# Performance work log

Hardware: AMD Instinct MI355X
Metric: run time of the kernel (lower is better)

Reference implementation:

```python
import jax, jax.numpy as jnp
import numpy as np

B, D, H = 1024, 1024, 4096  # batch, input_dim, hidden_dim
EPS = 1e-3  # keras LayerNormalization default epsilon


def layer_norm(x, gamma, beta):
    m = jnp.mean(x, axis=-1, keepdims=True)
    v = jnp.var(x, axis=-1, keepdims=True)
    return (x - m) * jax.lax.rsqrt(v + EPS) * gamma + beta


def setup_inputs() -> dict:
    key = jax.random.key(0)
    ks = jax.random.split(key, 8)
    C = D + H  # concat width for gate/FFN projections
    s_in = 0.02
    return {
        "x": jax.random.normal(ks[0], (B, D), jnp.float32),
        "hidden_state": jax.random.normal(ks[1], (B, H), jnp.float32),
        "W_u": jax.random.normal(ks[2], (C, H), jnp.float32) * s_in,
        "b_u": jnp.zeros((H,), jnp.float32),
        "W_r": jax.random.normal(ks[3], (C, H), jnp.float32) * s_in,
        "b_r": jnp.zeros((H,), jnp.float32),
        "W_g": jax.random.normal(ks[4], (C, H), jnp.float32) * s_in,
        "b_g": jnp.zeros((H,), jnp.float32),
        "W_up": jax.random.normal(ks[5], (C, H), jnp.float32) * s_in,
        "b_up": jnp.zeros((H,), jnp.float32),
        "W_d": jax.random.normal(ks[6], (H, D), jnp.float32) * s_in,
        "b_d": jnp.zeros((D,), jnp.float32),
        "gamma_h": jnp.ones((H,), jnp.float32),
        "beta_h": jnp.zeros((H,), jnp.float32),
        "gamma_o": jnp.ones((D,), jnp.float32),
        "beta_o": jnp.zeros((D,), jnp.float32),
    }


def reference(x, hidden_state, W_u, b_u, W_r, b_r, W_g, b_g, W_up, b_up,
              W_d, b_d, gamma_h, beta_h, gamma_o, beta_o):
    h = hidden_state
    combined = jnp.concatenate([x, h], axis=-1)          # [B, D+H]
    u = jax.nn.sigmoid(combined @ W_u + b_u)             # update gate [B, H]
    r = jax.nn.sigmoid(combined @ W_r + b_r)             # reset gate  [B, H]
    cand = jnp.concatenate([x, r * h], axis=-1)          # [B, D+H]
    gate = cand @ W_g + b_g
    up = cand @ W_up + b_up
    swiglu = jax.nn.silu(gate) * up                      # [B, H]
    new_h = layer_norm((1.0 - u) * h + u * swiglu + h, gamma_h, beta_h)
    out = layer_norm(new_h @ W_d + b_d, gamma_o, beta_o)  # [B, D]
    return out, new_h
```

## Files before the change

kernel.cpp:

```cpp
#include <hip/hip_runtime.h>
#include <hip/hip_bf16.h>
#include <math.h>


typedef unsigned short u16;
typedef unsigned int u32;
typedef __attribute__((ext_vector_type(8))) short short8;
typedef __attribute__((ext_vector_type(4))) float floatx4;

#define B_ROWS 1024
#define H_DIM 4096
#define D_DIM 1024
#define LDA_S 72

__device__ __forceinline__ float bf2f(u16 v) {
  u32 u = ((u32)v) << 16;
  return __builtin_bit_cast(float, u);
}
__device__ __forceinline__ u16 f2bf(float f) {
  u32 u = __builtin_bit_cast(u32, f);
  u32 r = (u + 0x7fffu + ((u >> 16) & 1u)) >> 16;
  return (u16)r;
}
__device__ __forceinline__ u32 pkbf(float lo, float hi) {
  return (u32)f2bf(lo) | ((u32)f2bf(hi) << 16);
}

__device__ __forceinline__ void gload_lds16(const u16* g, u16* l) {
  __builtin_amdgcn_global_load_lds(
      (const __attribute__((address_space(1))) void*)g,
      (__attribute__((address_space(3))) void*)l, 16, 0, 0);
}


__launch_bounds__(256)
__global__ void conv_w_k(const float* __restrict__ W0, const float* __restrict__ W1,
                         u16* __restrict__ img, int ldb, int KT, int nbHalf) {
  const int nb = blockIdx.x;
  const int kt = blockIdx.y;
  const float* W = (nb < nbHalf) ? W0 : W1;
  const int nbl = (nb < nbHalf) ? nb : (nb - nbHalf);
  const float* src = W + (size_t)kt * 64 * ldb + (size_t)nbl * 128;
  u16* dst = img + ((size_t)nb * KT + kt) * 8192;
  const int t = threadIdx.x;
  const int n = t & 127;
  const int half = t >> 7;
#pragma unroll
  for (int pass = 0; pass < 4; ++pass) {
    const int kc = half * 4 + pass;
    const float* sp = src + (size_t)(kc * 8) * ldb + n;
    uint4 o;
    o.x = pkbf(sp[0],                 sp[(size_t)ldb]);
    o.y = pkbf(sp[(size_t)2 * ldb],   sp[(size_t)3 * ldb]);
    o.z = pkbf(sp[(size_t)4 * ldb],   sp[(size_t)5 * ldb]);
    o.w = pkbf(sp[(size_t)6 * ldb],   sp[(size_t)7 * ldb]);
    *(uint4*)(dst + (size_t)(kc * 128 + n) * 8) = o;
  }
}

__launch_bounds__(256)
__global__ void conv_xh_k(const float* __restrict__ x, const float* __restrict__ h,
                          u16* __restrict__ imgX, u16* __restrict__ imgH) {
  const int kt = blockIdx.x;
  const int mb = blockIdx.y;
  const float* src;
  u16* dst;
  int lda;
  if (kt < 16) {
    lda = 1024;
    src = x + (size_t)mb * 128 * lda + (size_t)kt * 64;
    dst = imgX + ((size_t)mb * 16 + kt) * 8192;
  } else {
    lda = 4096;
    src = h + (size_t)mb * 128 * lda + (size_t)(kt - 16) * 64;
    dst = imgH + ((size_t)mb * 64 + (kt - 16)) * 8192;
  }
  const int t = threadIdx.x;
  const int j = t & 127;
  const int half = t >> 7;
  const float* sp = src + (size_t)j * lda + half * 32;
#pragma unroll
  for (int pass = 0; pass < 4; ++pass) {
    const int kc = half * 4 + pass;
    const float4 a = *(const float4*)(sp + pass * 8);
    const float4 b = *(const float4*)(sp + pass * 8 + 4);
    uint4 o;
    o.x = pkbf(a.x, a.y);
    o.y = pkbf(a.z, a.w);
    o.z = pkbf(b.x, b.y);
    o.w = pkbf(b.z, b.w);
    *(uint4*)(dst + (size_t)(kc * 128 + j) * 8) = o;
  }
}

template <int MODE>
__launch_bounds__(256)
__global__ void gemm_img(const u16* __restrict__ A0, const u16* __restrict__ A1,
                         const u16* __restrict__ Bimg,
                         const float* __restrict__ bias0, const float* __restrict__ bias1,
                         const float* __restrict__ hglob,
                         float* __restrict__ outF, u16* __restrict__ outB0,
                         u16* __restrict__ outB1) {
  constexpr int KT = (MODE == 3) ? 16 : 80;
  constexpr int KSPLIT = 16;
  constexpr int KT_B = (MODE == 3) ? 64 : 80;

  const int bx = blockIdx.x;
  const int by = blockIdx.y;
  const int kz = (MODE == 3) ? (int)blockIdx.z * 16 : 0;
  const int n0 = bx * 128;
  const int m0 = by * 128;
  const bool second = (MODE != 3) && (n0 >= 4096);
  const int ncol0 = second ? (n0 - 4096) : n0;

  __shared__ __align__(16) u16 As[2][8192];
  __shared__ __align__(16) u16 Bs[2][8192];

  const int t = threadIdx.x;
  const int w = t >> 6;
  const int lane = t & 63;
  const int q = lane >> 4;
  const int i16 = lane & 15;
  const int wm = (w >> 1) * 64;
  const int wn = (w & 1) * 64;

  floatx4 acc[4][4] = {};

  const u16* btile = Bimg + ((size_t)bx * KT_B + kz) * 8192;

  auto stage = [&](int kt, int buf) {
    const u16* a;
    if (MODE == 3) {
      a = A0 + ((size_t)by * 64 + kz + kt) * 8192;
    } else {
      a = (kt < KSPLIT) ? A0 + ((size_t)by * 16 + kt) * 8192
                        : A1 + ((size_t)by * 64 + (kt - KSPLIT)) * 8192;
    }
    const u16* b = btile + (size_t)kt * 8192;
    u16* As_ = &As[buf][0];
    u16* Bs_ = &Bs[buf][0];
#pragma unroll
    for (int i = 0; i < 4; ++i) {
      const int ch = (i * 4 + w) * 512;
      gload_lds16(a + ch + lane * 8, As_ + ch);
      gload_lds16(b + ch + lane * 8, Bs_ + ch);
    }
  };

  stage(0, 0);
  __syncthreads();
  int cur = 0;

  for (int kt = 0; kt < KT; ++kt) {
    if (kt + 1 < KT) stage(kt + 1, cur ^ 1);
#pragma unroll
    for (int s = 0; s < 2; ++s) {
      const int c = s * 4 + q;
      short8 av[4], bv[4];
#pragma unroll
      for (int tm = 0; tm < 4; ++tm)
        av[tm] = *(const short8*)(&As[cur][(size_t)(c * 128 + wm + tm * 16 + i16) * 8]);
#pragma unroll
      for (int tn = 0; tn < 4; ++tn)
        bv[tn] = *(const short8*)(&Bs[cur][(size_t)(c * 128 + wn + tn * 16 + i16) * 8]);
#pragma unroll
      for (int tm = 0; tm < 4; ++tm)
#pragma unroll
        for (int tn = 0; tn < 4; ++tn)
          acc[tm][tn] = __builtin_amdgcn_mfma_f32_16x16x32_bf16(av[tm], bv[tn], acc[tm][tn], 0, 0, 0);
    }
    __syncthreads();
    cur ^= 1;
  }

  const float* __restrict__ biasP = second ? bias1 : bias0;
  float* __restrict__ outP = (MODE == 3) ? outF + (size_t)blockIdx.z * (1024 * 1024) : outF;
#pragma unroll
  for (int tm = 0; tm < 4; ++tm) {
#pragma unroll
    for (int tn = 0; tn < 4; ++tn) {
      const int nloc = ncol0 + wn + tn * 16 + i16;
      const float b = (MODE == 3) ? 0.f : biasP[nloc];
      const int mbase = m0 + wm + tm * 16 + q * 4;
#pragma unroll
      for (int r = 0; r < 4; ++r) {
        const int m = mbase + r;
        const float v = acc[tm][tn][r] + b;
        if (MODE == 1) {
          const float sg = 1.f / (1.f + __expf(-v));
          if (!second) {
            outF[(size_t)m * 4096 + nloc] = sg;
          } else {
            const float rh = sg * hglob[(size_t)m * 4096 + nloc];
            const size_t tb = ((size_t)(m >> 7) * 64 + (nloc >> 6)) * 8192;
            outB0[tb + (size_t)((((nloc >> 3) & 7) * 128) + (m & 127)) * 8 + (nloc & 7)] = f2bf(rh);
          }
        } else if (MODE == 2) {
          if (!second) outB0[(size_t)m * 4096 + nloc] = f2bf(v);
          else         outB1[(size_t)m * 4096 + nloc] = f2bf(v);
        } else {
          outP[(size_t)m * 1024 + nloc] = v;
        }
      }
    }
  }
}

template <int MODE>
__launch_bounds__(256)
__global__ void gemm_k(const float* __restrict__ Af0, const float* __restrict__ Af1,
                       const u16* __restrict__ Ab,
                       const float* __restrict__ Bg0, const float* __restrict__ Bg1,
                       const float* __restrict__ bias0, const float* __restrict__ bias1,
                       const float* __restrict__ hglob,
                       float* __restrict__ outF, u16* __restrict__ outB0,
                       u16* __restrict__ outB1) {
  constexpr int K_TOT = (MODE == 3) ? 4096 : 5120;
  constexpr int KT = K_TOT / 64;
  constexpr int LDB = (MODE == 3) ? 1024 : 4096;

  const int n0 = blockIdx.x * 128;
  const int m0 = blockIdx.y * 128;
  const bool second = (MODE != 3) && (n0 >= 4096);
  const float* __restrict__ Bg = second ? Bg1 : Bg0;
  const int ncol0 = second ? (n0 - 4096) : n0;

  __shared__ __align__(16) u16 As[128 * LDA_S];
  __shared__ __align__(16) u16 Bs[64 * 128];

  const int t = threadIdx.x;
  const int w = t >> 6;
  const int lane = t & 63;
  const int q = lane >> 4;
  const int i16 = lane & 15;
  const int wm = (w >> 1) * 64;
  const int wn = (w & 1) * 64;

  floatx4 acc[4][4] = {};

  for (int kt = 0; kt < KT; ++kt) {
    const int k0 = kt * 64;
    const bool a_is_bf16 = (MODE == 2) && (k0 >= 1024);
    if (a_is_bf16) {
      const u16* Ag = Ab;
      const int lda = 4096;
      const int krel = k0 - 1024;
#pragma unroll
      for (int c = 0; c < 4; ++c) {
        const int p = c * 256 + t;
        const int row = p >> 3;
        const int cp = p & 7;
        const uint4 v = *(const uint4*)(Ag + (size_t)(m0 + row) * lda + krel + cp * 8);
        *(uint4*)(&As[row * LDA_S + cp * 8]) = v;
      }
    } else {
      const float* Ag;
      int lda, krel;
      if (MODE == 3)      { Ag = Af0; lda = 4096; krel = k0; }
      else if (k0 < 1024) { Ag = Af0; lda = 1024; krel = k0; }
      else                { Ag = Af1; lda = 4096; krel = k0 - 1024; }
#pragma unroll
      for (int c = 0; c < 8; ++c) {
        const int p = c * 256 + t;
        const int row = p >> 4;
        const int cp = p & 15;
        const float4 v = *(const float4*)(Ag + (size_t)(m0 + row) * lda + krel + cp * 4);
        ushort4 o;
        o.x = f2bf(v.x); o.y = f2bf(v.y); o.z = f2bf(v.z); o.w = f2bf(v.w);
        *(ushort4*)(&As[row * LDA_S + cp * 4]) = o;
      }
    }
#pragma unroll
    for (int cc = 0; cc < 2; ++cc) {
      const int c = 2 * w + cc;
      const float* bp = Bg + (size_t)(k0 + c * 8) * LDB + ncol0;
#pragma unroll
      for (int hn = 0; hn < 2; ++hn) {
        const int n = lane + hn * 64;
        const float* src = bp + n;
        u32 p0 = (u32)f2bf(src[0 * LDB]) | ((u32)f2bf(src[1 * LDB]) << 16);
        u32 p1 = (u32)f2bf(src[2 * LDB]) | ((u32)f2bf(src[3 * LDB]) << 16);
        u32 p2 = (u32)f2bf(src[4 * LDB]) | ((u32)f2bf(src[5 * LDB]) << 16);
        u32 p3 = (u32)f2bf(src[6 * LDB]) | ((u32)f2bf(src[7 * LDB]) << 16);
        *(uint4*)(&Bs[(size_t)(c * 128 + n) * 8]) = make_uint4(p0, p1, p2, p3);
      }
    }
    __syncthreads();
#pragma unroll
    for (int s = 0; s < 2; ++s) {
      short8 av[4], bv[4];
#pragma unroll
      for (int tm = 0; tm < 4; ++tm) {
        const int r = wm + tm * 16 + i16;
        av[tm] = *(const short8*)(&As[r * LDA_S + (s * 4 + q) * 8]);
      }
#pragma unroll
      for (int tn = 0; tn < 4; ++tn) {
        const int n = wn + tn * 16 + i16;
        const int c = s * 4 + q;
        bv[tn] = *(const short8*)(&Bs[(size_t)(c * 128 + n) * 8]);
      }
#pragma unroll
      for (int tm = 0; tm < 4; ++tm)
#pragma unroll
        for (int tn = 0; tn < 4; ++tn)
          acc[tm][tn] = __builtin_amdgcn_mfma_f32_16x16x32_bf16(av[tm], bv[tn], acc[tm][tn], 0, 0, 0);
    }
    __syncthreads();
  }

  const float* __restrict__ biasP = second ? bias1 : bias0;
  constexpr int LDO = (MODE == 3) ? 1024 : 4096;
#pragma unroll
  for (int tm = 0; tm < 4; ++tm) {
#pragma unroll
    for (int tn = 0; tn < 4; ++tn) {
      const int nloc = ncol0 + wn + tn * 16 + i16;
      const float b = biasP[nloc];
      const int mbase = m0 + wm + tm * 16 + q * 4;
#pragma unroll
      for (int r = 0; r < 4; ++r) {
        const int m = mbase + r;
        const float v = acc[tm][tn][r] + b;
        const size_t oidx = (size_t)m * LDO + nloc;
        if (MODE == 1) {
          const float sg = 1.f / (1.f + __expf(-v));
          if (!second) outF[oidx] = sg;
          else         outB0[oidx] = f2bf(sg * hglob[oidx]);
        } else if (MODE == 2) {
          if (!second) outB0[oidx] = f2bf(v);
          else         outB1[oidx] = f2bf(v);
        } else {
          outF[oidx] = v;
        }
      }
    }
  }
}

__launch_bounds__(256)
__global__ void ln_h_k(const float* u_f, const u16* __restrict__ wsg,
                       const u16* __restrict__ wsup, const float* __restrict__ h,
                       const float* __restrict__ gamma, const float* __restrict__ beta,
                       float* out, u16* __restrict__ imgNH) {
  const int row = blockIdx.x, t = threadIdx.x;
  const size_t base = (size_t)row * H_DIM;
  const int i0 = t * 16;
  float tv[16];
  float s = 0.f, s2 = 0.f;
#pragma unroll
  for (int j = 0; j < 16; ++j) {
    const int idx = i0 + j;
    const float u = u_f[base + idx];
    const float g = bf2f(wsg[base + idx]);
    const float up = bf2f(wsup[base + idx]);
    const float hh = h[base + idx];
    const float sw = (g / (1.f + __expf(-g))) * up;
    const float x = (2.f - u) * hh + u * sw;
    tv[j] = x; s += x; s2 += x * x;
  }
#pragma unroll
  for (int off = 32; off; off >>= 1) {
    s += __shfl_down(s, off);
    s2 += __shfl_down(s2, off);
  }
  __shared__ float red[8];
  const int w = t >> 6, lane = t & 63;
  if (lane == 0) { red[w] = s; red[4 + w] = s2; }
  __syncthreads();
  const float S = red[0] + red[1] + red[2] + red[3];
  const float S2 = red[4] + red[5] + red[6] + red[7];
  const float mean = S * (1.f / (float)H_DIM);
  const float var = fmaxf(S2 * (1.f / (float)H_DIM) - mean * mean, 0.f);
  const float rstd = rsqrtf(var + 1e-3f);
#pragma unroll
  for (int cc = 0; cc < 2; ++cc) {
    float o[8];
#pragma unroll
    for (int jj = 0; jj < 8; ++jj) {
      const int idx = i0 + cc * 8 + jj;
      o[jj] = (tv[cc * 8 + jj] - mean) * rstd * gamma[idx] + beta[idx];
      out[base + idx] = o[jj];
    }
    if (imgNH) {
      const int idx8 = i0 + cc * 8;
      uint4 v;
      v.x = pkbf(o[0], o[1]);
      v.y = pkbf(o[2], o[3]);
      v.z = pkbf(o[4], o[5]);
      v.w = pkbf(o[6], o[7]);
      *(uint4*)(&imgNH[((size_t)(row >> 7) * 64 + (idx8 >> 6)) * 8192 +
                       (size_t)((((idx8 >> 3) & 7) * 128) + (row & 127)) * 8]) = v;
    }
  }
}

__launch_bounds__(256)
__global__ void ln_o_k(const float* __restrict__ part, const float* __restrict__ bias,
                       const float* __restrict__ gamma, const float* __restrict__ beta,
                       float* __restrict__ out) {
  const int row = blockIdx.x, t = threadIdx.x;
  const size_t base = (size_t)row * D_DIM;
  const int i0 = t * 4;
  constexpr size_t PSTRIDE = (size_t)1024 * 1024;
  float tv[4];
  float s = 0.f, s2 = 0.f;
#pragma unroll
  for (int j = 0; j < 4; ++j) {
    const size_t idx = base + i0 + j;
    const float x = part[idx] + part[idx + PSTRIDE] + part[idx + 2 * PSTRIDE] +
                    part[idx + 3 * PSTRIDE] + bias[i0 + j];
    tv[j] = x; s += x; s2 += x * x;
  }
#pragma unroll
  for (int off = 32; off; off >>= 1) {
    s += __shfl_down(s, off);
    s2 += __shfl_down(s2, off);
  }
  __shared__ float red[8];
  const int w = t >> 6, lane = t & 63;
  if (lane == 0) { red[w] = s; red[4 + w] = s2; }
  __syncthreads();
  const float S = red[0] + red[1] + red[2] + red[3];
  const float S2 = red[4] + red[5] + red[6] + red[7];
  const float mean = S * (1.f / (float)D_DIM);
  const float var = fmaxf(S2 * (1.f / (float)D_DIM) - mean * mean, 0.f);
  const float rstd = rsqrtf(var + 1e-3f);
#pragma unroll
  for (int j = 0; j < 4; ++j) {
    const int idx = i0 + j;
    out[base + idx] = (tv[j] - mean) * rstd * gamma[idx] + beta[idx];
  }
}

__launch_bounds__(256)
__global__ void ln_o_fb(float* io, const float* __restrict__ gamma,
                        const float* __restrict__ beta) {
  const int row = blockIdx.x, t = threadIdx.x;
  const size_t base = (size_t)row * D_DIM;
  const int i0 = t * 4;
  float tv[4];
  float s = 0.f, s2 = 0.f;
#pragma unroll
  for (int j = 0; j < 4; ++j) {
    const float x = io[base + i0 + j];
    tv[j] = x; s += x; s2 += x * x;
  }
#pragma unroll
  for (int off = 32; off; off >>= 1) {
    s += __shfl_down(s, off);
    s2 += __shfl_down(s2, off);
  }
  __shared__ float red[8];
  const int w = t >> 6, lane = t & 63;
  if (lane == 0) { red[w] = s; red[4 + w] = s2; }
  __syncthreads();
  const float S = red[0] + red[1] + red[2] + red[3];
  const float S2 = red[4] + red[5] + red[6] + red[7];
  const float mean = S * (1.f / (float)D_DIM);
  const float var = fmaxf(S2 * (1.f / (float)D_DIM) - mean * mean, 0.f);
  const float rstd = rsqrtf(var + 1e-3f);
#pragma unroll
  for (int j = 0; j < 4; ++j) {
    const int idx = i0 + j;
    io[base + idx] = (tv[j] - mean) * rstd * gamma[idx] + beta[idx];
  }
}

extern "C" void kernel_launch(void* const* d_in, const int* in_sizes, int n_in,
                              void* d_out, int out_size, void* d_ws, size_t ws_size,
                              hipStream_t stream) {
  (void)in_sizes; (void)n_in; (void)out_size;
  const float* x       = (const float*)d_in[0];
  const float* h       = (const float*)d_in[1];
  const float* W_u     = (const float*)d_in[2];
  const float* b_u     = (const float*)d_in[3];
  const float* W_r     = (const float*)d_in[4];
  const float* b_r     = (const float*)d_in[5];
  const float* W_g     = (const float*)d_in[6];
  const float* b_g     = (const float*)d_in[7];
  const float* W_up    = (const float*)d_in[8];
  const float* b_up    = (const float*)d_in[9];
  const float* W_d     = (const float*)d_in[10];
  const float* b_d     = (const float*)d_in[11];
  const float* gamma_h = (const float*)d_in[12];
  const float* beta_h  = (const float*)d_in[13];
  const float* gamma_o = (const float*)d_in[14];
  const float* beta_o  = (const float*)d_in[15];

  float* out_final = (float*)d_out;
  float* out_newh  = (float*)d_out + (size_t)B_ROWS * D_DIM;
  float* u_buf = out_newh;
  float* o_pre = out_final;

  dim3 blk(256);

  const size_t SZ_W  = (size_t)64 * 80 * 16384;
  const size_t SZ_X  = (size_t)8 * 16 * 16384;
  const size_t SZ_H  = (size_t)8 * 64 * 16384;
  const size_t SZ_RH = SZ_H;
  const size_t SZ_G  = (size_t)B_ROWS * H_DIM * 2;
  const size_t SZ_UP = SZ_G;
  const size_t NEED  = SZ_W + SZ_X + SZ_H + SZ_RH + SZ_G + SZ_UP;

  if (ws_size >= NEED) {
    char* ws = (char*)d_ws;
    u16* imgW  = (u16*)(ws);
    u16* imgX  = (u16*)(ws + SZ_W);
    u16* imgH  = (u16*)(ws + SZ_W + SZ_X);
    u16* imgNH = imgH;
    u16* imgRH = (u16*)(ws + SZ_W + SZ_X + SZ_H);
    u16* ws_g  = (u16*)(ws + SZ_W + SZ_X + SZ_H + SZ_RH);
    u16* ws_up = (u16*)(ws + SZ_W + SZ_X + SZ_H + SZ_RH + SZ_G);
    float* part = (float*)ws_g;

    conv_xh_k<<<dim3(80, 8), blk, 0, stream>>>(x, h, imgX, imgH);
    conv_w_k<<<dim3(64, 80), blk, 0, stream>>>(W_u, W_r, imgW, 4096, 80, 32);
    gemm_img<1><<<dim3(64, 8), blk, 0, stream>>>(imgX, imgH, imgW, b_u, b_r, h,
                                                 u_buf, imgRH, nullptr);
    conv_w_k<<<dim3(64, 80), blk, 0, stream>>>(W_g, W_up, imgW, 4096, 80, 32);
    gemm_img<2><<<dim3(64, 8), blk, 0, stream>>>(imgX, imgRH, imgW, b_g, b_up, nullptr,
                                                 nullptr, ws_g, ws_up);
    ln_h_k<<<dim3(B_ROWS), blk, 0, stream>>>(u_buf, ws_g, ws_up, h, gamma_h, beta_h,
                                             out_newh, imgNH);
    conv_w_k<<<dim3(8, 64), blk, 0, stream>>>(W_d, nullptr, imgW, 1024, 64, 8);
    gemm_img<3><<<dim3(8, 8, 4), blk, 0, stream>>>(imgNH, imgNH, imgW, nullptr, nullptr,
                                                   nullptr, part, nullptr, nullptr);
    ln_o_k<<<dim3(B_ROWS), blk, 0, stream>>>(part, b_d, gamma_o, beta_o, out_final);
  } else {
    char* ws = (char*)d_ws;
    u16* ws_rh = (u16*)(ws);
    u16* ws_g  = (u16*)(ws + (size_t)8 * 1024 * 1024);
    u16* ws_up = (u16*)(ws + (size_t)16 * 1024 * 1024);

    gemm_k<1><<<dim3(64, 8), blk, 0, stream>>>(x, h, nullptr, W_u, W_r, b_u, b_r, h,
                                               u_buf, ws_rh, nullptr);
    gemm_k<2><<<dim3(64, 8), blk, 0, stream>>>(x, nullptr, ws_rh, W_g, W_up, b_g, b_up,
                                               nullptr, nullptr, ws_g, ws_up);
    ln_h_k<<<dim3(B_ROWS), blk, 0, stream>>>(u_buf, ws_g, ws_up, h, gamma_h, beta_h,
                                             out_newh, nullptr);
    gemm_k<3><<<dim3(8, 8), blk, 0, stream>>>(out_newh, nullptr, nullptr, W_d, nullptr,
                                              b_d, nullptr, nullptr, o_pre, nullptr, nullptr);
    ln_o_fb<<<dim3(B_ROWS), blk, 0, stream>>>(o_pre, gamma_o, beta_o);
  }
}
```

Before: 643.5 us.

## Overlap next weight conversion with current GEMM via combined launches

Adds a gemm_conv kernel whose grid holds both the GEMM tiles and extra blocks that convert the next stage's fp32 weights to the bf16 tiled image. A second weight buffer lets the W_g/W_up and W_d conversions run alongside the gate GEMMs instead of as separate serialized launches. The weight-conversion body is also rewritten to read float2 pairs and write two 16-byte chunks per thread for wider memory access. The new path needs twice the weight workspace and falls back to the old sequence otherwise. Conversion blocks compete with GEMM blocks for CUs and bandwidth.

```diff
diff --git a/kernel.cpp b/kernel.cpp
--- a/kernel.cpp
+++ b/kernel.cpp
@@ -32,30 +32,40 @@
       (__attribute__((address_space(3))) void*)l, 16, 0, 0);
 }
 
-
-__launch_bounds__(256)
-__global__ void conv_w_k(const float* __restrict__ W0, const float* __restrict__ W1,
-                         u16* __restrict__ img, int ldb, int KT, int nbHalf) {
-  const int nb = blockIdx.x;
-  const int kt = blockIdx.y;
+__device__ __forceinline__ void conv_w_body(int nb, int kt,
+                                            const float* __restrict__ W0,
+                                            const float* __restrict__ W1,
+                                            u16* __restrict__ img, int ldb,
+                                            int KT, int nbHalf) {
   const float* W = (nb < nbHalf) ? W0 : W1;
   const int nbl = (nb < nbHalf) ? nb : (nb - nbHalf);
   const float* src = W + (size_t)kt * 64 * ldb + (size_t)nbl * 128;
   u16* dst = img + ((size_t)nb * KT + kt) * 8192;
   const int t = threadIdx.x;
-  const int n = t & 127;
-  const int half = t >> 7;
-#pragma unroll
-  for (int pass = 0; pass < 4; ++pass) {
-    const int kc = half * 4 + pass;
-    const float* sp = src + (size_t)(kc * 8) * ldb + n;
-    uint4 o;
-    o.x = pkbf(sp[0],                 sp[(size_t)ldb]);
-    o.y = pkbf(sp[(size_t)2 * ldb],   sp[(size_t)3 * ldb]);
-    o.z = pkbf(sp[(size_t)4 * ldb],   sp[(size_t)5 * ldb]);
-    o.w = pkbf(sp[(size_t)6 * ldb],   sp[(size_t)7 * ldb]);
-    *(uint4*)(dst + (size_t)(kc * 128 + n) * 8) = o;
-  }
+  const int n2 = (t & 63) * 2;
+  const int kcg = t >> 6;
+#pragma unroll
+  for (int kk = 0; kk < 2; ++kk) {
+    const int kc = kcg * 2 + kk;
+    const float* sp = src + (size_t)(kc * 8) * ldb + n2;
+    float2 r[8];
+#pragma unroll
+    for (int c = 0; c < 8; ++c) r[c] = *(const float2*)(sp + (size_t)c * ldb);
+    uint4 o0, o1;
+    o0.x = pkbf(r[0].x, r[1].x); o0.y = pkbf(r[2].x, r[3].x);
+    o0.z = pkbf(r[4].x, r[5].x); o0.w = pkbf(r[6].x, r[7].x);
+    o1.x = pkbf(r[0].y, r[1].y); o1.y = pkbf(r[2].y, r[3].y);
+    o1.z = pkbf(r[4].y, r[5].y); o1.w = pkbf(r[6].y, r[7].y);
+    u16* dp = dst + (size_t)(kc * 128 + n2) * 8;
+    *(uint4*)(dp) = o0;
+    *(uint4*)(dp + 8) = o1;
+  }
+}
+
+__launch_bounds__(256)
+__global__ void conv_w_k(const float* __restrict__ W0, const float* __restrict__ W1,
+                         u16* __restrict__ img, int ldb, int KT, int nbHalf) {
+  conv_w_body(blockIdx.x, blockIdx.y, W0, W1, img, ldb, KT, nbHalf);
 }
 
 __launch_bounds__(256)
@@ -90,6 +100,109 @@
     o.z = pkbf(b.x, b.y);
     o.w = pkbf(b.z, b.w);
     *(uint4*)(dst + (size_t)(kc * 128 + j) * 8) = o;
+  }
+}
+
+template <int MODE>
+__launch_bounds__(256)
+__global__ void gemm_conv(const u16* __restrict__ A0, const u16* __restrict__ A1,
+                          const u16* __restrict__ Bimg,
+                          const float* __restrict__ bias0, const float* __restrict__ bias1,
+                          const float* __restrict__ hglob,
+                          float* __restrict__ outF, u16* __restrict__ outB0,
+                          u16* __restrict__ outB1, int ngemm,
+                          const float* __restrict__ cW0, const float* __restrict__ cW1,
+                          u16* __restrict__ cimg, int cldb, int cKT, int cnbHalf,
+                          int csh) {
+  __shared__ __align__(16) u16 As[8192];
+  __shared__ __align__(16) u16 Bs[8192];
+
+  const int fid = blockIdx.x;
+  if (fid >= ngemm) {
+    const int cid = fid - ngemm;
+    conv_w_body(cid & ((1 << csh) - 1), cid >> csh, cW0, cW1, cimg, cldb, cKT, cnbHalf);
+    return;
+  }
+
+  constexpr int KT = 80;
+  constexpr int KSPLIT = 16;
+
+  const int bx = fid & 63;
+  const int by = fid >> 6;
+  const int n0 = bx * 128;
+  const int m0 = by * 128;
+  const bool second = (n0 >= 4096);
+  const int ncol0 = second ? (n0 - 4096) : n0;
+
+  const int t = threadIdx.x;
+  const int w = t >> 6;
+  const int lane = t & 63;
+  const int q = lane >> 4;
+  const int i16 = lane & 15;
+  const int wm = (w >> 1) * 64;
+  const int wn = (w & 1) * 64;
+
+  floatx4 acc[4][4] = {};
+
+  const u16* btile = Bimg + (size_t)bx * KT * 8192;
+
+  for (int kt = 0; kt < KT; ++kt) {
+    const u16* a = (kt < KSPLIT) ? A0 + ((size_t)by * 16 + kt) * 8192
+                                 : A1 + ((size_t)by * 64 + (kt - KSPLIT)) * 8192;
+    const u16* b = btile + (size_t)kt * 8192;
+#pragma unroll
+    for (int i = 0; i < 4; ++i) {
+      const int ch = (i * 4 + w) * 512;
+      gload_lds16(a + ch + lane * 8, &As[ch]);
+      gload_lds16(b + ch + lane * 8, &Bs[ch]);
+    }
+    __syncthreads();
+#pragma unroll
+    for (int s = 0; s < 2; ++s) {
+      const int c = s * 4 + q;
+      short8 av[4], bv[4];
+#pragma unroll
+      for (int tm = 0; tm < 4; ++tm)
+        av[tm] = *(const short8*)(&As[(size_t)(c * 128 + wm + tm * 16 + i16) * 8]);
+#pragma unroll
+      for (int tn = 0; tn < 4; ++tn)
+        bv[tn] = *(const short8*)(&Bs[(size_t)(c * 128 + wn + tn * 16 + i16) * 8]);
+#pragma unroll
+      for (int tm = 0; tm < 4; ++tm)
+#pragma unroll
+        for (int tn = 0; tn < 4; ++tn)
+          acc[tm][tn] = __builtin_amdgcn_mfma_f32_16x16x32_bf16(av[tm], bv[tn], acc[tm][tn], 0, 0, 0);
+    }
+    __syncthreads();
+  }
+
+  const float* __restrict__ biasP = second ? bias1 : bias0;
+#pragma unroll
+  for (int tm = 0; tm < 4; ++tm) {
+#pragma unroll
+    for (int tn = 0; tn < 4; ++tn) {
+      const int nloc = ncol0 + wn + tn * 16 + i16;
+      const float b = biasP[nloc];
+      const int mbase = m0 + wm + tm * 16 + q * 4;
+#pragma unroll
+      for (int r = 0; r < 4; ++r) {
+        const int m = mbase + r;
+        const float v = acc[tm][tn][r] + b;
+        if (MODE == 1) {
+          const float sg = 1.f / (1.f + __expf(-v));
+          if (!second) {
+            outF[(size_t)m * 4096 + nloc] = sg;
+          } else {
+            const float rh = sg * hglob[(size_t)m * 4096 + nloc];
+            const size_t tb = ((size_t)(m >> 7) * 64 + (nloc >> 6)) * 8192;
+            outB0[tb + (size_t)((((nloc >> 3) & 7) * 128) + (m & 127)) * 8 + (nloc & 7)] = f2bf(rh);
+          }
+        } else {
+          if (!second) outB0[(size_t)m * 4096 + nloc] = f2bf(v);
+          else         outB1[(size_t)m * 4096 + nloc] = f2bf(v);
+        }
+      }
+    }
   }
 }
 
@@ -495,15 +608,42 @@
 
   dim3 blk(256);
 
-  const size_t SZ_W  = (size_t)64 * 80 * 16384;
-  const size_t SZ_X  = (size_t)8 * 16 * 16384;
-  const size_t SZ_H  = (size_t)8 * 64 * 16384;
-  const size_t SZ_RH = SZ_H;
-  const size_t SZ_G  = (size_t)B_ROWS * H_DIM * 2;
-  const size_t SZ_UP = SZ_G;
-  const size_t NEED  = SZ_W + SZ_X + SZ_H + SZ_RH + SZ_G + SZ_UP;
-
-  if (ws_size >= NEED) {
+  const size_t MiB = 1024 * 1024;
+  const size_t SZ_W  = 80 * MiB;
+  const size_t SZ_X  = 2 * MiB;
+  const size_t SZ_H  = 8 * MiB;
+  const size_t SZ_RH = 8 * MiB;
+  const size_t SZ_G  = 8 * MiB;
+  const size_t SZ_UP = 8 * MiB;
+  const size_t NEED_SEQ   = SZ_W + SZ_X + SZ_H + SZ_RH + SZ_G + SZ_UP;
+  const size_t NEED_FUSED = 2 * SZ_W + SZ_X + SZ_H + SZ_RH + SZ_G + SZ_UP;
+
+  if (ws_size >= NEED_FUSED) {
+    char* ws = (char*)d_ws;
+    u16* imgWA = (u16*)(ws);
+    u16* imgWB = (u16*)(ws + SZ_W);
+    u16* imgX  = (u16*)(ws + 2 * SZ_W);
+    u16* imgH  = (u16*)(ws + 2 * SZ_W + SZ_X);
+    u16* imgNH = imgH;
+    u16* imgRH = (u16*)(ws + 2 * SZ_W + SZ_X + SZ_H);
+    u16* ws_g  = (u16*)(ws + 2 * SZ_W + SZ_X + SZ_H + SZ_RH);
+    u16* ws_up = (u16*)(ws + 2 * SZ_W + SZ_X + SZ_H + SZ_RH + SZ_G);
+    float* part = (float*)ws_g;
+
+    conv_xh_k<<<dim3(80, 8), blk, 0, stream>>>(x, h, imgX, imgH);
+    conv_w_k<<<dim3(64, 80), blk, 0, stream>>>(W_u, W_r, imgWA, 4096, 80, 32);
+    gemm_conv<1><<<dim3(512 + 5120), blk, 0, stream>>>(
+        imgX, imgH, imgWA, b_u, b_r, h, u_buf, imgRH, nullptr, 512,
+        W_g, W_up, imgWB, 4096, 80, 32, 6);
+    gemm_conv<2><<<dim3(512 + 512), blk, 0, stream>>>(
+        imgX, imgRH, imgWB, b_g, b_up, nullptr, nullptr, ws_g, ws_up, 512,
+        W_d, nullptr, imgWA, 1024, 64, 8, 3);
+    ln_h_k<<<dim3(B_ROWS), blk, 0, stream>>>(u_buf, ws_g, ws_up, h, gamma_h, beta_h,
+                                             out_newh, imgNH);
+    gemm_img<3><<<dim3(8, 8, 4), blk, 0, stream>>>(imgNH, imgNH, imgWA, nullptr, nullptr,
+                                                   nullptr, part, nullptr, nullptr);
+    ln_o_k<<<dim3(B_ROWS), blk, 0, stream>>>(part, b_d, gamma_o, beta_o, out_final);
+  } else if (ws_size >= NEED_SEQ) {
     char* ws = (char*)d_ws;
     u16* imgW  = (u16*)(ws);
     u16* imgX  = (u16*)(ws + SZ_W);
@@ -530,8 +670,8 @@
   } else {
     char* ws = (char*)d_ws;
     u16* ws_rh = (u16*)(ws);
-    u16* ws_g  = (u16*)(ws + (size_t)8 * 1024 * 1024);
-    u16* ws_up = (u16*)(ws + (size_t)16 * 1024 * 1024);
+    u16* ws_g  = (u16*)(ws + (size_t)8 * MiB);
+    u16* ws_up = (u16*)(ws + (size_t)16 * MiB);
 
     gemm_k<1><<<dim3(64, 8), blk, 0, stream>>>(x, h, nullptr, W_u, W_r, b_u, b_r, h,
                                                u_buf, ws_rh, nullptr);
```

Measured after the change: 618.1 us. 3.9% less time.
